# Performance work log

Measured on AMD Instinct MI355X. Metric: run time of the kernel, lower is better.

## Reference

```python
import jax, jax.numpy as jnp
import numpy as np

EPSILON = 0.3
ALPHA = 0.7
LN_EPS = 1e-5


def _layernorm(x, g, b):
    mu = jnp.mean(x, axis=-1, keepdims=True)
    var = jnp.mean((x - mu) ** 2, axis=-1, keepdims=True)
    return (x - mu) / jnp.sqrt(var + LN_EPS) * g + b


def setup_inputs() -> dict:
    key = jax.random.key(0)
    ks = jax.random.split(key, 6)
    B, N, D, L = 1, 2048, 768, 16
    s = 0.05  # weight scale to keep sigmoid/exp well-conditioned
    return {
        "x": jax.random.normal(ks[0], (B, N, D), jnp.float32),
        "proj_w": jax.random.normal(ks[1], (D, L), jnp.float32) * s,
        "proj_b": jnp.zeros((L,), jnp.float32),
        "ln1_g": jnp.ones((L,), jnp.float32),
        "ln1_b": jnp.zeros((L,), jnp.float32),
        "pi_w1": jax.random.normal(ks[2], (L, D), jnp.float32) * s,
        "pi_b1": jnp.zeros((D,), jnp.float32),
        "pi_w2": jax.random.normal(ks[3], (D, 1), jnp.float32) * s,
        "pi_b2": jnp.zeros((1,), jnp.float32),
        "dt": jnp.full((1,), 0.05, jnp.float32),
        "f_w": jax.random.normal(ks[4], (D, D), jnp.float32) * s,
        "f_b": jnp.zeros((D,), jnp.float32),
        "ln2_g": jnp.ones((D,), jnp.float32),
        "ln2_b": jnp.zeros((D,), jnp.float32),
    }


def reference(x, proj_w, proj_b, ln1_g, ln1_b, pi_w1, pi_b1, pi_w2, pi_b2, dt, f_w, f_b, ln2_g, ln2_b):
    B, N, D = x.shape
    # proj_list: Linear -> LayerNorm -> ReLU. [B,N,L]
    x_proj = jax.nn.relu(_layernorm(x @ proj_w + proj_b, ln1_g, ln1_b))
    # RBF kernel over pairwise differences. [B,N,N]
    diff = x_proj[:, :, None, :] - x_proj[:, None, :, :]
    K_eps = jnp.exp(-(1.0 / (4.0 * EPSILON)) * jnp.sum(diff * diff, axis=-1))
    q_tilde = jnp.sum(K_eps, axis=2)  # [B,N]
    # pi_list: Linear -> ReLU -> Linear -> Sigmoid. [B,N]
    pi = jax.nn.sigmoid(jax.nn.relu(x_proj @ pi_w1 + pi_b1) @ pi_w2 + pi_b2)[..., 0]
    v = pi / q_tilde  # diagonal of D_epsilon_tilde
    # K_tilde = K_eps @ diag(v): column scaling (math-equivalent to bmm with diag_embed)
    K_tilde = K_eps * v[:, None, :]
    d = jnp.sum(K_tilde, axis=2) + 1e-5  # diagonal of D_tilde
    # inv(D_tilde) @ K_tilde: row scaling; then subtract identity
    L_op = (1.0 / EPSILON) * (K_tilde / d[:, :, None]) - jnp.eye(N, dtype=x.dtype)[None]
    L_mat = L_op[0]  # .squeeze(0), B == 1
    # f(x): modeled as linear map
    target = x @ f_w + f_b  # [B,N,D]
    tt = dt * jnp.einsum('ij,bjd->bid', L_mat, target)  # target_transformed
    target1 = target + tt
    target2 = ALPHA * x + (1.0 - ALPHA) * (target1 + tt)
    return _layernorm(target2, ln2_g, ln2_b)
```

## Files before the change

kernel.cpp:

```cpp
#include <hip/hip_runtime.h>
#include <math.h>

#define EPSILON 0.3f
#define ALPHA 0.7f
#define LN_EPS 1e-5f

typedef __bf16 bf16x8 __attribute__((ext_vector_type(8)));
typedef float f32x4 __attribute__((ext_vector_type(4)));

__device__ __forceinline__ unsigned short f2bf(float f) {
  unsigned int u = __float_as_uint(f);
  return (unsigned short)((u + 0x7fffu + ((u >> 16) & 1u)) >> 16);
}
__device__ __forceinline__ unsigned int pack2(float lo, float hi) {
  return (unsigned int)f2bf(lo) | ((unsigned int)f2bf(hi) << 16);
}

__device__ __forceinline__ void async16(const unsigned short* g,
                                        unsigned short* l) {
  __builtin_amdgcn_global_load_lds(
      (const __attribute__((address_space(1))) unsigned int*)g,
      (__attribute__((address_space(3))) unsigned int*)l, 16, 0, 0);
}

__device__ __forceinline__ float wave_reduce(float v) {
#pragma unroll
  for (int off = 32; off > 0; off >>= 1) v += __shfl_xor(v, off, 64);
  return v;
}

__device__ __forceinline__ float blk_reduce_sum(float v, float* red) {
  v = wave_reduce(v);
  int lane = threadIdx.x & 63, wid = threadIdx.x >> 6;
  __syncthreads();
  if (lane == 0) red[wid] = v;
  __syncthreads();
  return red[0] + red[1] + red[2] + red[3];
}

__global__ __launch_bounds__(256) void k_proj(
    const float* __restrict__ x, const float* __restrict__ proj_w,
    const float* __restrict__ proj_b, const float* __restrict__ ln1_g,
    const float* __restrict__ ln1_b, const float* __restrict__ pi_w1,
    const float* __restrict__ pi_b1, const float* __restrict__ pi_w2,
    const float* __restrict__ pi_b2, const float* __restrict__ fw,
    unsigned short* __restrict__ fwTb, float* __restrict__ xp,
    float* __restrict__ s, float* __restrict__ pi, int N, int D) {
  __shared__ float xs[16][68];
  __shared__ float ws[64][20];
  __shared__ float ysh[16][17];
  __shared__ float xps[16][16];
  __shared__ float pr[16][4];
  int tid = threadIdx.x;
  int nProj = N / 16;
  if (blockIdx.x >= (unsigned)nProj) {
    unsigned short(*tile)[33] = (unsigned short(*)[33])&ws[0][0];
    int t = blockIdx.x - nProj;
    int tx = tid & 31, ty = tid >> 5;
    int cols = D / 32;
    int c0 = (t % cols) * 32, r0 = (t / cols) * 32;
#pragma unroll
    for (int i = 0; i < 4; ++i) {
      int r = r0 + ty + i * 8;
      tile[ty + i * 8][tx] = f2bf(fw[(size_t)r * D + c0 + tx]);
    }
    __syncthreads();
#pragma unroll
    for (int i = 0; i < 4; ++i) {
      int cc = c0 + ty + i * 8;
      fwTb[(size_t)cc * D + r0 + tx] = tile[tx][ty + i * 8];
    }
    return;
  }
  int row0 = blockIdx.x * 16;
  int row = tid >> 4, l = tid & 15;
  int lane = tid & 63, w = tid >> 6;
  int skc = (tid & 15) * 4;
  int wk = tid >> 2, wl = (tid & 3) * 4;
  float acc = 0.f;
  for (int k0 = 0; k0 < D; k0 += 64) {
    float4 xv = *(const float4*)(x + (size_t)(row0 + row) * D + k0 + skc);
    float4 wv = *(const float4*)(proj_w + (size_t)(k0 + wk) * 16 + wl);
    __syncthreads();
    *(float4*)&xs[row][skc] = xv;
    *(float4*)&ws[wk][wl] = wv;
    __syncthreads();
#pragma unroll
    for (int kk = 0; kk < 64; kk += 4) {
      float4 a4 = *(const float4*)&xs[row][kk];
      acc += a4.x * ws[kk + 0][l];
      acc += a4.y * ws[kk + 1][l];
      acc += a4.z * ws[kk + 2][l];
      acc += a4.w * ws[kk + 3][l];
    }
  }
  float y = acc + proj_b[l];
  ysh[row][l] = y;
  __syncthreads();
  float mu = 0.f;
#pragma unroll
  for (int t = 0; t < 16; ++t) mu += ysh[row][t];
  mu *= (1.f / 16.f);
  float var = 0.f;
#pragma unroll
  for (int t = 0; t < 16; ++t) { float d2 = ysh[row][t] - mu; var += d2 * d2; }
  var *= (1.f / 16.f);
  float rstd = rsqrtf(var + LN_EPS);
  float xpv = fmaxf((y - mu) * rstd * ln1_g[l] + ln1_b[l], 0.f);
  xps[row][l] = xpv;
  xp[(size_t)(row0 + row) * 16 + l] = xpv;
  float sq = xpv * xpv;
  sq += __shfl_xor(sq, 8, 64);
  sq += __shfl_xor(sq, 4, 64);
  sq += __shfl_xor(sq, 2, 64);
  sq += __shfl_xor(sq, 1, 64);
  if ((lane & 15) == 0) s[row0 + row] = sq;
  __syncthreads();
  float w1r[3][16], b1r[3], w2r[3];
#pragma unroll
  for (int c = 0; c < 3; ++c) {
    int d0 = tid + c * 256;
    b1r[c] = pi_b1[d0];
    w2r[c] = pi_w2[d0];
#pragma unroll
    for (int t = 0; t < 16; ++t) w1r[c][t] = pi_w1[(size_t)t * D + d0];
  }
#pragma unroll
  for (int r = 0; r < 16; ++r) {
    float xv[16];
#pragma unroll
    for (int t4 = 0; t4 < 4; ++t4) {
      float4 xq = *(const float4*)&xps[r][t4 * 4];
      xv[t4 * 4 + 0] = xq.x; xv[t4 * 4 + 1] = xq.y;
      xv[t4 * 4 + 2] = xq.z; xv[t4 * 4 + 3] = xq.w;
    }
    float pa = 0.f;
#pragma unroll
    for (int c = 0; c < 3; ++c) {
      float h = b1r[c];
#pragma unroll
      for (int t = 0; t < 16; ++t) h += xv[t] * w1r[c][t];
      h = fmaxf(h, 0.f);
      pa += h * w2r[c];
    }
    float pv = wave_reduce(pa);
    if (lane == 0) pr[r][w] = pv;
  }
  __syncthreads();
  if (tid < 16) {
    float tot = pr[tid][0] + pr[tid][1] + pr[tid][2] + pr[tid][3] + pi_b2[0];
    pi[row0 + tid] = 1.f / (1.f + expf(-tot));
  }
}

__global__ __launch_bounds__(256) void k_keps(
    const float* __restrict__ xp, const float* __restrict__ s,
    const float* __restrict__ pi, unsigned short* __restrict__ Kb,
    float* __restrict__ v, int N) {
  __shared__ float qs[4][4];
  int i0 = blockIdx.x * 4;
  int tid = threadIdx.x, lane = tid & 63, w = tid >> 6;
  float a[4][16], si[4];
#pragma unroll
  for (int r = 0; r < 4; ++r) {
    const float* ap = xp + (size_t)(i0 + r) * 16;
#pragma unroll
    for (int t = 0; t < 16; ++t) a[r][t] = ap[t];
    si[r] = s[i0 + r];
  }
  const float c = 1.f / (4.f * EPSILON);
  float qa[4] = {0.f, 0.f, 0.f, 0.f};
  for (int it = 0; it < N / 512; ++it) {
    int j = it * 512 + tid * 2;
    const float4* bp = (const float4*)(xp + (size_t)j * 16);
    float4 b0 = bp[0], b1 = bp[1], b2 = bp[2], b3 = bp[3];
    float4 c0 = bp[4], c1 = bp[5], c2 = bp[6], c3 = bp[7];
    float bv[16] = {b0.x, b0.y, b0.z, b0.w, b1.x, b1.y, b1.z, b1.w,
                    b2.x, b2.y, b2.z, b2.w, b3.x, b3.y, b3.z, b3.w};
    float cv[16] = {c0.x, c0.y, c0.z, c0.w, c1.x, c1.y, c1.z, c1.w,
                    c2.x, c2.y, c2.z, c2.w, c3.x, c3.y, c3.z, c3.w};
    float sj0 = s[j], sj1 = s[j + 1];
#pragma unroll
    for (int r = 0; r < 4; ++r) {
      float d0 = 0.f, d1 = 0.f;
#pragma unroll
      for (int t = 0; t < 16; ++t) { d0 += a[r][t] * bv[t]; d1 += a[r][t] * cv[t]; }
      float k0 = __expf(-c * (si[r] + sj0 - 2.f * d0));
      float k1 = __expf(-c * (si[r] + sj1 - 2.f * d1));
      *(unsigned int*)(Kb + (size_t)(i0 + r) * N + j) = pack2(k0, k1);
      qa[r] += k0 + k1;
    }
  }
#pragma unroll
  for (int r = 0; r < 4; ++r) {
    float t = wave_reduce(qa[r]);
    if (lane == 0) qs[r][w] = t;
  }
  __syncthreads();
  if (tid < 4) {
    float tot = qs[tid][0] + qs[tid][1] + qs[tid][2] + qs[tid][3];
    v[i0 + tid] = pi[i0 + tid] / tot;
  }
}

__global__ __launch_bounds__(256) void k_prep(
    const unsigned short* __restrict__ Kb, const float* __restrict__ v,
    float* __restrict__ dv, const float* __restrict__ x,
    unsigned short* __restrict__ xvbT, int N, int D) {
  __shared__ float sh[544];
  int bid = blockIdx.x, tid = threadIdx.x;
  if (bid < N) {
    int i = bid;
    float acc = 0.f;
    for (int j8 = tid * 8; j8 < N; j8 += 256 * 8) {
      uint4 kv4 = *(const uint4*)(Kb + (size_t)i * N + j8);
      float4 va = *(const float4*)(v + j8);
      float4 vb = *(const float4*)(v + j8 + 4);
      unsigned int u;
      u = kv4.x;
      acc += __uint_as_float(u << 16) * va.x + __uint_as_float(u & 0xffff0000u) * va.y;
      u = kv4.y;
      acc += __uint_as_float(u << 16) * va.z + __uint_as_float(u & 0xffff0000u) * va.w;
      u = kv4.z;
      acc += __uint_as_float(u << 16) * vb.x + __uint_as_float(u & 0xffff0000u) * vb.y;
      u = kv4.w;
      acc += __uint_as_float(u << 16) * vb.z + __uint_as_float(u & 0xffff0000u) * vb.w;
    }
    float tot = blk_reduce_sum(acc, sh);
    if (tid == 0) dv[i] = tot + 1e-5f;
  } else {
    int t = bid - N;
    unsigned short(*tile)[33] = (unsigned short(*)[33])sh;
    int tx = tid & 31, ty = tid >> 5;
    int cols = D / 32;
    int c0 = (t % cols) * 32;
    int r0 = (t / cols) * 32;
#pragma unroll
    for (int i = 0; i < 4; ++i) {
      int r = r0 + ty + i * 8;
      tile[ty + i * 8][tx] = f2bf(v[r] * x[(size_t)r * D + c0 + tx]);
    }
    __syncthreads();
#pragma unroll
    for (int i = 0; i < 4; ++i) {
      int cc = c0 + ty + i * 8;
      xvbT[(size_t)cc * N + r0 + tx] = tile[tx][ty + i * 8];
    }
  }
}

#define GEMM_KLOOP(Aptr, Bptr, Kdim)                                          \
  int tid = threadIdx.x;                                                      \
  int w = tid >> 6, l = tid & 63;                                             \
  int ln = l & 15, quad = l >> 4;                                             \
  int mh = (w & 1) * 32, nh = (w >> 1) * 32;                                  \
  int row0 = blockIdx.y * 64, col0 = blockIdx.x * 64;                         \
  int srow = w * 4 + (l >> 4);                                                \
  int swz = ((l & 15) ^ srow) * 8;                                            \
  const unsigned short* gA = Aptr + (size_t)(row0 + srow) * Kdim + swz;       \
  const unsigned short* gB = Bptr + (size_t)(col0 + srow) * Kdim + swz;       \
  f32x4 acc[2][2] = {};                                                       \
  for (int k0 = 0; k0 < Kdim; k0 += 128) {                                    \
    __syncthreads();                                                          \
    _Pragma("unroll")                                                         \
    for (int q = 0; q < 4; ++q) {                                             \
      async16(gA + (size_t)q * 16 * Kdim + k0, As + (q * 16 + w * 4) * 128);  \
      async16(gB + (size_t)q * 16 * Kdim + k0, Bs + (q * 16 + w * 4) * 128);  \
    }                                                                         \
    __syncthreads();                                                          \
    _Pragma("unroll")                                                         \
    for (int ks = 0; ks < 4; ++ks) {                                          \
      bf16x8 bfr[2], afr[2];                                                  \
      _Pragma("unroll")                                                       \
      for (int nt = 0; nt < 2; ++nt) {                                        \
        int r = nh + nt * 16 + ln;                                            \
        int cix = (ks * 4 + quad) ^ (r & 15);                                 \
        bfr[nt] = *(const bf16x8*)&Bs[r * 128 + cix * 8];                     \
      }                                                                       \
      _Pragma("unroll")                                                       \
      for (int mt = 0; mt < 2; ++mt) {                                        \
        int r = mh + mt * 16 + ln;                                            \
        int cix = (ks * 4 + quad) ^ (r & 15);                                 \
        afr[mt] = *(const bf16x8*)&As[r * 128 + cix * 8];                     \
      }                                                                       \
      _Pragma("unroll")                                                       \
      for (int mt = 0; mt < 2; ++mt)                                          \
        _Pragma("unroll")                                                     \
        for (int nt = 0; nt < 2; ++nt)                                        \
          acc[mt][nt] = __builtin_amdgcn_mfma_f32_16x16x32_bf16(              \
              afr[mt], bfr[nt], acc[mt][nt], 0, 0, 0);                        \
    }                                                                         \
  }

__global__ __launch_bounds__(256) void k_gemmA(
    const unsigned short* __restrict__ A, const unsigned short* __restrict__ Bt,
    const float* __restrict__ x, const float* __restrict__ dv,
    const float* __restrict__ dtp, unsigned short* __restrict__ Z,
    int M, int N, int K) {
  __shared__ unsigned short As[64 * 128];
  __shared__ unsigned short Bs[64 * 128];
  GEMM_KLOOP(A, Bt, K)
  float dtv = dtp[0];
  float c2 = (1.f - ALPHA) * (1.f - 2.f * dtv);
  float c3b = (1.f - ALPHA) * 2.f * dtv / EPSILON;
#pragma unroll
  for (int mt = 0; mt < 2; ++mt)
#pragma unroll
    for (int nt = 0; nt < 2; ++nt) {
      int col = col0 + nh + nt * 16 + ln;
#pragma unroll
      for (int r = 0; r < 4; ++r) {
        int row = row0 + mh + mt * 16 + quad * 4 + r;
        float c3 = c3b / dv[row];
        Z[(size_t)row * N + col] =
            f2bf(c2 * x[(size_t)row * N + col] + c3 * acc[mt][nt][r]);
      }
    }
}

__global__ __launch_bounds__(256) void k_gemmB(
    const unsigned short* __restrict__ A, const unsigned short* __restrict__ Bt,
    const float* __restrict__ x, const float* __restrict__ bias,
    const float* __restrict__ dtp, float* __restrict__ out,
    int M, int N, int K) {
  __shared__ unsigned short As[64 * 128];
  __shared__ unsigned short Bs[64 * 128];
  GEMM_KLOOP(A, Bt, K)
  float dtv = dtp[0];
  float cb = (1.f - ALPHA) * (1.f - 2.f * dtv) +
             (1.f - ALPHA) * 2.f * dtv / EPSILON;
#pragma unroll
  for (int mt = 0; mt < 2; ++mt)
#pragma unroll
    for (int nt = 0; nt < 2; ++nt) {
      int col = col0 + nh + nt * 16 + ln;
      float bv = cb * bias[col];
#pragma unroll
      for (int r = 0; r < 4; ++r) {
        int row = row0 + mh + mt * 16 + quad * 4 + r;
        size_t idx = (size_t)row * N + col;
        out[idx] = ALPHA * x[idx] + acc[mt][nt][r] + bv;
      }
    }
}

__global__ __launch_bounds__(256) void k_ln_rows(
    float* __restrict__ out, const float* __restrict__ g,
    const float* __restrict__ b, int D) {
  __shared__ float red[4];
  int i = blockIdx.x, tid = threadIdx.x;
  float vv[4];
  int nt = D / 256;
  float sum = 0.f;
  for (int t = 0; t < nt; ++t) {
    vv[t] = out[(size_t)i * D + tid + t * 256];
    sum += vv[t];
  }
  float mu = blk_reduce_sum(sum, red) / (float)D;
  float sq = 0.f;
  for (int t = 0; t < nt; ++t) { float d2 = vv[t] - mu; sq += d2 * d2; }
  float var = blk_reduce_sum(sq, red) / (float)D;
  float rs = rsqrtf(var + LN_EPS);
  for (int t = 0; t < nt; ++t) {
    int d0 = tid + t * 256;
    out[(size_t)i * D + d0] = (vv[t] - mu) * rs * g[d0] + b[d0];
  }
}

extern "C" void kernel_launch(void* const* d_in, const int* in_sizes, int n_in,
                              void* d_out, int out_size, void* d_ws, size_t ws_size,
                              hipStream_t stream) {
  const float* x = (const float*)d_in[0];
  const float* proj_w = (const float*)d_in[1];
  const float* proj_b = (const float*)d_in[2];
  const float* ln1_g = (const float*)d_in[3];
  const float* ln1_b = (const float*)d_in[4];
  const float* pi_w1 = (const float*)d_in[5];
  const float* pi_b1 = (const float*)d_in[6];
  const float* pi_w2 = (const float*)d_in[7];
  const float* pi_b2 = (const float*)d_in[8];
  const float* dt = (const float*)d_in[9];
  const float* f_w = (const float*)d_in[10];
  const float* f_b = (const float*)d_in[11];
  const float* ln2_g = (const float*)d_in[12];
  const float* ln2_b = (const float*)d_in[13];
  float* out = (float*)d_out;

  int D = in_sizes[11];
  int N = in_sizes[0] / D;

  unsigned short* Kb = (unsigned short*)d_ws;
  unsigned short* xvbT = Kb + (size_t)N * N;
  unsigned short* fwTb = xvbT + (size_t)D * N;
  unsigned short* Z = fwTb + (size_t)D * D;
  float* xp = (float*)(Z + (size_t)N * D);
  float* s = xp + (size_t)N * 16;
  float* pi = s + N;
  float* v = pi + N;
  float* dv = v + N;

  int fwB = (D / 32) * (D / 32);
  int xvtB = (D / 32) * (N / 32);

  k_proj<<<N / 16 + fwB, 256, 0, stream>>>(x, proj_w, proj_b, ln1_g, ln1_b,
                                           pi_w1, pi_b1, pi_w2, pi_b2, f_w,
                                           fwTb, xp, s, pi, N, D);
  k_keps<<<N / 4, 256, 0, stream>>>(xp, s, pi, Kb, v, N);
  k_prep<<<N + xvtB, 256, 0, stream>>>(Kb, v, dv, x, xvbT, N, D);
  k_gemmA<<<dim3(D / 64, N / 64), 256, 0, stream>>>(Kb, xvbT, x, dv, dt, Z,
                                                    N, D, N);
  k_gemmB<<<dim3(D / 64, N / 64), 256, 0, stream>>>(Z, fwTb, x, f_b, dt, out,
                                                    N, D, D);
  k_ln_rows<<<N, 256, 0, stream>>>(out, ln2_g, ln2_b, D);
}
```

Before: 158.4 us.

## Fuse six kernels into one persistent cooperative kernel with grid syncs

Replaces the six separate kernel launches with a single cooperative persistent kernel that loops over work items in each stage and separates stages with grid-wide syncs. This removes per-launch overhead and inter-kernel gaps. In exchange, the grid is capped at 512 blocks (bounded by occupancy), so the large stages run in grid-stride loops and may lose parallelism. Grid syncs also add their own cost, and the original kernels are kept as a fallback if the cooperative launch fails.

```diff
diff --git a/kernel.cpp b/kernel.cpp
--- a/kernel.cpp
+++ b/kernel.cpp
@@ -1,5 +1,8 @@
 #include <hip/hip_runtime.h>
+#include <hip/hip_cooperative_groups.h>
 #include <math.h>
+
+namespace cg = cooperative_groups;
 
 #define EPSILON 0.3f
 #define ALPHA 0.7f
@@ -37,6 +40,424 @@
   __syncthreads();
   return red[0] + red[1] + red[2] + red[3];
 }
+
+struct ProjSh {
+  float xs[16][68];
+  float ws[64][20];
+  float ysh[16][17];
+  float xps[16][16];
+  float pr[16][4];
+};
+
+__global__ __launch_bounds__(256) void k_mega(
+    const float* __restrict__ x, const float* __restrict__ proj_w,
+    const float* __restrict__ proj_b, const float* __restrict__ ln1_g,
+    const float* __restrict__ ln1_b, const float* __restrict__ pi_w1,
+    const float* __restrict__ pi_b1, const float* __restrict__ pi_w2,
+    const float* __restrict__ pi_b2, const float* __restrict__ dtp,
+    const float* __restrict__ fw, const float* __restrict__ fb,
+    const float* __restrict__ ln2_g, const float* __restrict__ ln2_b,
+    unsigned short* __restrict__ Kb, unsigned short* __restrict__ xvbT,
+    unsigned short* __restrict__ fwTb, unsigned short* __restrict__ Z,
+    float* __restrict__ xp, float* __restrict__ s, float* __restrict__ pi,
+    float* __restrict__ v, float* __restrict__ dv, float* __restrict__ out,
+    int N, int D) {
+  cg::grid_group gg = cg::this_grid();
+  __shared__ __align__(16) unsigned char pool[32768];
+  __shared__ float qs[4][4];
+  const int tid = threadIdx.x;
+  const int bid = blockIdx.x;
+  const int nBlk = gridDim.x;
+  const int lane = tid & 63, wv = tid >> 6;
+
+  {
+    int nProj = N / 16;
+    int cols = D / 64;
+    int nItems = nProj + cols * cols;
+    for (int item = bid; item < nItems; item += nBlk) {
+      __syncthreads();
+      if (item >= nProj) {
+        int t = item - nProj;
+        unsigned short(*tile)[65] = (unsigned short(*)[65])pool;
+        int c0 = (t % cols) * 64, r0 = (t / cols) * 64;
+#pragma unroll
+        for (int i = 0; i < 16; ++i) {
+          int rr = wv * 16 + i;
+          tile[rr][lane] = f2bf(fw[(size_t)(r0 + rr) * D + c0 + lane]);
+        }
+        __syncthreads();
+#pragma unroll
+        for (int i = 0; i < 16; ++i) {
+          int rr = wv * 16 + i;
+          fwTb[(size_t)(c0 + rr) * D + r0 + lane] = tile[lane][rr];
+        }
+        continue;
+      }
+      ProjSh& P = *(ProjSh*)pool;
+      int row0 = item * 16;
+      int row = tid >> 4, l = tid & 15;
+      int skc = (tid & 15) * 4;
+      int wk = tid >> 2, wl = (tid & 3) * 4;
+      float acc = 0.f;
+      for (int k0 = 0; k0 < D; k0 += 64) {
+        float4 xv = *(const float4*)(x + (size_t)(row0 + row) * D + k0 + skc);
+        float4 wvec = *(const float4*)(proj_w + (size_t)(k0 + wk) * 16 + wl);
+        __syncthreads();
+        *(float4*)&P.xs[row][skc] = xv;
+        *(float4*)&P.ws[wk][wl] = wvec;
+        __syncthreads();
+#pragma unroll
+        for (int kk = 0; kk < 64; kk += 4) {
+          float4 a4 = *(const float4*)&P.xs[row][kk];
+          acc += a4.x * P.ws[kk + 0][l];
+          acc += a4.y * P.ws[kk + 1][l];
+          acc += a4.z * P.ws[kk + 2][l];
+          acc += a4.w * P.ws[kk + 3][l];
+        }
+      }
+      float y = acc + proj_b[l];
+      P.ysh[row][l] = y;
+      __syncthreads();
+      float mu = 0.f;
+#pragma unroll
+      for (int t = 0; t < 16; ++t) mu += P.ysh[row][t];
+      mu *= (1.f / 16.f);
+      float var = 0.f;
+#pragma unroll
+      for (int t = 0; t < 16; ++t) {
+        float d2 = P.ysh[row][t] - mu;
+        var += d2 * d2;
+      }
+      var *= (1.f / 16.f);
+      float rstd = rsqrtf(var + LN_EPS);
+      float xpv = fmaxf((y - mu) * rstd * ln1_g[l] + ln1_b[l], 0.f);
+      P.xps[row][l] = xpv;
+      xp[(size_t)(row0 + row) * 16 + l] = xpv;
+      float sq = xpv * xpv;
+      sq += __shfl_xor(sq, 8, 64);
+      sq += __shfl_xor(sq, 4, 64);
+      sq += __shfl_xor(sq, 2, 64);
+      sq += __shfl_xor(sq, 1, 64);
+      if ((lane & 15) == 0) s[row0 + row] = sq;
+      __syncthreads();
+      float w1r[3][16], b1r[3], w2r[3];
+#pragma unroll
+      for (int c = 0; c < 3; ++c) {
+        int d0 = tid + c * 256;
+        b1r[c] = pi_b1[d0];
+        w2r[c] = pi_w2[d0];
+#pragma unroll
+        for (int t = 0; t < 16; ++t) w1r[c][t] = pi_w1[(size_t)t * D + d0];
+      }
+#pragma unroll
+      for (int r = 0; r < 16; ++r) {
+        float xv2[16];
+#pragma unroll
+        for (int t4 = 0; t4 < 4; ++t4) {
+          float4 xq = *(const float4*)&P.xps[r][t4 * 4];
+          xv2[t4 * 4 + 0] = xq.x;
+          xv2[t4 * 4 + 1] = xq.y;
+          xv2[t4 * 4 + 2] = xq.z;
+          xv2[t4 * 4 + 3] = xq.w;
+        }
+        float pa = 0.f;
+#pragma unroll
+        for (int c = 0; c < 3; ++c) {
+          float h = b1r[c];
+#pragma unroll
+          for (int t = 0; t < 16; ++t) h += xv2[t] * w1r[c][t];
+          h = fmaxf(h, 0.f);
+          pa += h * w2r[c];
+        }
+        float pv = wave_reduce(pa);
+        if (lane == 0) P.pr[r][wv] = pv;
+      }
+      __syncthreads();
+      if (tid < 16) {
+        float tot = P.pr[tid][0] + P.pr[tid][1] + P.pr[tid][2] + P.pr[tid][3] +
+                    pi_b2[0];
+        pi[row0 + tid] = 1.f / (1.f + expf(-tot));
+      }
+    }
+  }
+  __threadfence();
+  gg.sync();
+
+  {
+    int nItems = N / 4;
+    for (int item = bid; item < nItems; item += nBlk) {
+      __syncthreads();
+      int i0 = item * 4;
+      float a[4][16], si[4];
+#pragma unroll
+      for (int r = 0; r < 4; ++r) {
+        const float* ap = xp + (size_t)(i0 + r) * 16;
+#pragma unroll
+        for (int t = 0; t < 16; ++t) a[r][t] = ap[t];
+        si[r] = s[i0 + r];
+      }
+      const float cc = 1.f / (4.f * EPSILON);
+      float qa[4] = {0.f, 0.f, 0.f, 0.f};
+      for (int it = 0; it < N / 512; ++it) {
+        int j = it * 512 + tid * 2;
+        const float4* bp = (const float4*)(xp + (size_t)j * 16);
+        float4 b0 = bp[0], b1 = bp[1], b2 = bp[2], b3 = bp[3];
+        float4 c0 = bp[4], c1 = bp[5], c2 = bp[6], c3 = bp[7];
+        float bvv[16] = {b0.x, b0.y, b0.z, b0.w, b1.x, b1.y, b1.z, b1.w,
+                         b2.x, b2.y, b2.z, b2.w, b3.x, b3.y, b3.z, b3.w};
+        float cvv[16] = {c0.x, c0.y, c0.z, c0.w, c1.x, c1.y, c1.z, c1.w,
+                         c2.x, c2.y, c2.z, c2.w, c3.x, c3.y, c3.z, c3.w};
+        float sj0 = s[j], sj1 = s[j + 1];
+#pragma unroll
+        for (int r = 0; r < 4; ++r) {
+          float d0 = 0.f, d1 = 0.f;
+#pragma unroll
+          for (int t = 0; t < 16; ++t) {
+            d0 += a[r][t] * bvv[t];
+            d1 += a[r][t] * cvv[t];
+          }
+          float k0 = __expf(-cc * (si[r] + sj0 - 2.f * d0));
+          float k1 = __expf(-cc * (si[r] + sj1 - 2.f * d1));
+          *(unsigned int*)(Kb + (size_t)(i0 + r) * N + j) = pack2(k0, k1);
+          qa[r] += k0 + k1;
+        }
+      }
+#pragma unroll
+      for (int r = 0; r < 4; ++r) {
+        float t = wave_reduce(qa[r]);
+        if (lane == 0) qs[r][wv] = t;
+      }
+      __syncthreads();
+      if (tid < 4) {
+        float tot = qs[tid][0] + qs[tid][1] + qs[tid][2] + qs[tid][3];
+        v[i0 + tid] = pi[i0 + tid] / tot;
+      }
+    }
+  }
+  __threadfence();
+  gg.sync();
+
+  {
+    int nDv = N / 4;
+    int cols = D / 64;
+    int nXT = cols * (N / 64);
+    for (int item = bid; item < nDv + nXT; item += nBlk) {
+      if (item < nDv) {
+        int i = item * 4 + wv;
+        const unsigned short* kr = Kb + (size_t)i * N;
+        float acc = 0.f;
+        for (int c0 = lane * 8; c0 < N; c0 += 512) {
+          uint4 kv = *(const uint4*)(kr + c0);
+          float4 va = *(const float4*)(v + c0);
+          float4 vb = *(const float4*)(v + c0 + 4);
+          unsigned int u;
+          u = kv.x;
+          acc += __uint_as_float(u << 16) * va.x +
+                 __uint_as_float(u & 0xffff0000u) * va.y;
+          u = kv.y;
+          acc += __uint_as_float(u << 16) * va.z +
+                 __uint_as_float(u & 0xffff0000u) * va.w;
+          u = kv.z;
+          acc += __uint_as_float(u << 16) * vb.x +
+                 __uint_as_float(u & 0xffff0000u) * vb.y;
+          u = kv.w;
+          acc += __uint_as_float(u << 16) * vb.z +
+                 __uint_as_float(u & 0xffff0000u) * vb.w;
+        }
+        acc = wave_reduce(acc);
+        if (lane == 0) dv[i] = acc + 1e-5f;
+      } else {
+        int t = item - nDv;
+        __syncthreads();
+        unsigned short(*tile)[65] = (unsigned short(*)[65])pool;
+        int c0 = (t % cols) * 64, r0 = (t / cols) * 64;
+#pragma unroll
+        for (int i = 0; i < 16; ++i) {
+          int rr = wv * 16 + i;
+          tile[rr][lane] =
+              f2bf(v[r0 + rr] * x[(size_t)(r0 + rr) * D + c0 + lane]);
+        }
+        __syncthreads();
+#pragma unroll
+        for (int i = 0; i < 16; ++i) {
+          int rr = wv * 16 + i;
+          xvbT[(size_t)(c0 + rr) * N + r0 + lane] = tile[lane][rr];
+        }
+      }
+    }
+  }
+  __threadfence();
+  gg.sync();
+
+  {
+    float dtv = dtp[0];
+    float c2 = (1.f - ALPHA) * (1.f - 2.f * dtv);
+    float c3b = (1.f - ALPHA) * 2.f * dtv / EPSILON;
+    unsigned short* As = (unsigned short*)pool;
+    unsigned short* Bs = As + 64 * 128;
+    int tilesX = D / 64;
+    int nT = tilesX * (N / 64);
+    int ln = lane & 15, quad = lane >> 4;
+    int mh = (wv & 1) * 32, nh = (wv >> 1) * 32;
+    int srow = wv * 4 + quad;
+    int swz = (ln ^ srow) * 8;
+    for (int item = bid; item < nT; item += nBlk) {
+      int row0 = (item / tilesX) * 64, col0 = (item % tilesX) * 64;
+      const unsigned short* gA = Kb + (size_t)(row0 + srow) * N + swz;
+      const unsigned short* gB = xvbT + (size_t)(col0 + srow) * N + swz;
+      f32x4 acc[2][2] = {};
+      for (int k0 = 0; k0 < N; k0 += 128) {
+        __syncthreads();
+#pragma unroll
+        for (int q = 0; q < 4; ++q) {
+          async16(gA + (size_t)q * 16 * N + k0, As + (q * 16 + wv * 4) * 128);
+          async16(gB + (size_t)q * 16 * N + k0, Bs + (q * 16 + wv * 4) * 128);
+        }
+        __syncthreads();
+#pragma unroll
+        for (int ks = 0; ks < 4; ++ks) {
+          bf16x8 bfr[2], afr[2];
+#pragma unroll
+          for (int nt = 0; nt < 2; ++nt) {
+            int r = nh + nt * 16 + ln;
+            int cix = (ks * 4 + quad) ^ (r & 15);
+            bfr[nt] = *(const bf16x8*)&Bs[r * 128 + cix * 8];
+          }
+#pragma unroll
+          for (int mt = 0; mt < 2; ++mt) {
+            int r = mh + mt * 16 + ln;
+            int cix = (ks * 4 + quad) ^ (r & 15);
+            afr[mt] = *(const bf16x8*)&As[r * 128 + cix * 8];
+          }
+#pragma unroll
+          for (int mt = 0; mt < 2; ++mt)
+#pragma unroll
+            for (int nt = 0; nt < 2; ++nt)
+              acc[mt][nt] = __builtin_amdgcn_mfma_f32_16x16x32_bf16(
+                  afr[mt], bfr[nt], acc[mt][nt], 0, 0, 0);
+        }
+      }
+#pragma unroll
+      for (int mt = 0; mt < 2; ++mt)
+#pragma unroll
+        for (int nt = 0; nt < 2; ++nt) {
+          int col = col0 + nh + nt * 16 + ln;
+#pragma unroll
+          for (int r = 0; r < 4; ++r) {
+            int row = row0 + mh + mt * 16 + quad * 4 + r;
+            float c3 = c3b / dv[row];
+            Z[(size_t)row * D + col] =
+                f2bf(c2 * x[(size_t)row * D + col] + c3 * acc[mt][nt][r]);
+          }
+        }
+    }
+  }
+  __threadfence();
+  gg.sync();
+
+  {
+    float dtv = dtp[0];
+    float cb = (1.f - ALPHA) * (1.f - 2.f * dtv) +
+               (1.f - ALPHA) * 2.f * dtv / EPSILON;
+    unsigned short* As = (unsigned short*)pool;
+    unsigned short* Bs = As + 64 * 128;
+    int tilesX = D / 64;
+    int nT = tilesX * (N / 64);
+    int ln = lane & 15, quad = lane >> 4;
+    int mh = (wv & 1) * 32, nh = (wv >> 1) * 32;
+    int srow = wv * 4 + quad;
+    int swz = (ln ^ srow) * 8;
+    for (int item = bid; item < nT; item += nBlk) {
+      int row0 = (item / tilesX) * 64, col0 = (item % tilesX) * 64;
+      const unsigned short* gA = Z + (size_t)(row0 + srow) * D + swz;
+      const unsigned short* gB = fwTb + (size_t)(col0 + srow) * D + swz;
+      f32x4 acc[2][2] = {};
+      for (int k0 = 0; k0 < D; k0 += 128) {
+        __syncthreads();
+#pragma unroll
+        for (int q = 0; q < 4; ++q) {
+          async16(gA + (size_t)q * 16 * D + k0, As + (q * 16 + wv * 4) * 128);
+          async16(gB + (size_t)q * 16 * D + k0, Bs + (q * 16 + wv * 4) * 128);
+        }
+        __syncthreads();
+#pragma unroll
+        for (int ks = 0; ks < 4; ++ks) {
+          bf16x8 bfr[2], afr[2];
+#pragma unroll
+          for (int nt = 0; nt < 2; ++nt) {
+            int r = nh + nt * 16 + ln;
+            int cix = (ks * 4 + quad) ^ (r & 15);
+            bfr[nt] = *(const bf16x8*)&Bs[r * 128 + cix * 8];
+          }
+#pragma unroll
+          for (int mt = 0; mt < 2; ++mt) {
+            int r = mh + mt * 16 + ln;
+            int cix = (ks * 4 + quad) ^ (r & 15);
+            afr[mt] = *(const bf16x8*)&As[r * 128 + cix * 8];
+          }
+#pragma unroll
+          for (int mt = 0; mt < 2; ++mt)
+#pragma unroll
+            for (int nt = 0; nt < 2; ++nt)
+              acc[mt][nt] = __builtin_amdgcn_mfma_f32_16x16x32_bf16(
+                  afr[mt], bfr[nt], acc[mt][nt], 0, 0, 0);
+        }
+      }
+#pragma unroll
+      for (int mt = 0; mt < 2; ++mt)
+#pragma unroll
+        for (int nt = 0; nt < 2; ++nt) {
+          int col = col0 + nh + nt * 16 + ln;
+          float bv = cb * fb[col];
+#pragma unroll
+          for (int r = 0; r < 4; ++r) {
+            int row = row0 + mh + mt * 16 + quad * 4 + r;
+            size_t idx = (size_t)row * D + col;
+            out[idx] = ALPHA * x[idx] + acc[mt][nt][r] + bv;
+          }
+        }
+    }
+  }
+  __threadfence();
+  gg.sync();
+
+  {
+    int nItems = N / 4;
+    for (int item = bid; item < nItems; item += nBlk) {
+      int i = item * 4 + wv;
+      float4 vv[3];
+      float sum = 0.f;
+#pragma unroll
+      for (int t = 0; t < 3; ++t) {
+        vv[t] = *(const float4*)(out + (size_t)i * D + lane * 4 + t * 256);
+        sum += vv[t].x + vv[t].y + vv[t].z + vv[t].w;
+      }
+      float mu = wave_reduce(sum) / (float)D;
+      float sq = 0.f;
+#pragma unroll
+      for (int t = 0; t < 3; ++t) {
+        float dx = vv[t].x - mu, dy = vv[t].y - mu;
+        float dz = vv[t].z - mu, dw = vv[t].w - mu;
+        sq += dx * dx + dy * dy + dz * dz + dw * dw;
+      }
+      float var = wave_reduce(sq) / (float)D;
+      float rs = rsqrtf(var + LN_EPS);
+#pragma unroll
+      for (int t = 0; t < 3; ++t) {
+        int d0 = lane * 4 + t * 256;
+        float4 gv = *(const float4*)(ln2_g + d0);
+        float4 bv = *(const float4*)(ln2_b + d0);
+        float4 o;
+        o.x = (vv[t].x - mu) * rs * gv.x + bv.x;
+        o.y = (vv[t].y - mu) * rs * gv.y + bv.y;
+        o.z = (vv[t].z - mu) * rs * gv.z + bv.z;
+        o.w = (vv[t].w - mu) * rs * gv.w + bv.w;
+        *(float4*)(out + (size_t)i * D + d0) = o;
+      }
+    }
+  }
+}
+
 
 __global__ __launch_bounds__(256) void k_proj(
     const float* __restrict__ x, const float* __restrict__ proj_w,
@@ -399,17 +820,41 @@
   float* v = pi + N;
   float* dv = v + N;
 
-  int fwB = (D / 32) * (D / 32);
-  int xvtB = (D / 32) * (N / 32);
-
-  k_proj<<<N / 16 + fwB, 256, 0, stream>>>(x, proj_w, proj_b, ln1_g, ln1_b,
-                                           pi_w1, pi_b1, pi_w2, pi_b2, f_w,
-                                           fwTb, xp, s, pi, N, D);
-  k_keps<<<N / 4, 256, 0, stream>>>(xp, s, pi, Kb, v, N);
-  k_prep<<<N + xvtB, 256, 0, stream>>>(Kb, v, dv, x, xvbT, N, D);
-  k_gemmA<<<dim3(D / 64, N / 64), 256, 0, stream>>>(Kb, xvbT, x, dv, dt, Z,
-                                                    N, D, N);
-  k_gemmB<<<dim3(D / 64, N / 64), 256, 0, stream>>>(Z, fwTb, x, f_b, dt, out,
-                                                    N, D, D);
-  k_ln_rows<<<N, 256, 0, stream>>>(out, ln2_g, ln2_b, D);
-}
+  bool ok = false;
+  int maxBlk = 0;
+  hipError_t qerr =
+      hipOccupancyMaxActiveBlocksPerMultiprocessor(&maxBlk, k_mega, 256, 0);
+  if (qerr == hipSuccess && maxBlk > 0) {
+    int dev = 0, numCU = 256;
+    hipGetDevice(&dev);
+    hipDeviceGetAttribute(&numCU, hipDeviceAttributeMultiprocessorCount, dev);
+    long cap = (long)maxBlk * (long)numCU;
+    int grid = (int)(cap < 512 ? cap : 512);
+    void* kargs[] = {(void*)&x,     (void*)&proj_w, (void*)&proj_b,
+                     (void*)&ln1_g, (void*)&ln1_b,  (void*)&pi_w1,
+                     (void*)&pi_b1, (void*)&pi_w2,  (void*)&pi_b2,
+                     (void*)&dt,    (void*)&f_w,    (void*)&f_b,
+                     (void*)&ln2_g, (void*)&ln2_b,  (void*)&Kb,
+                     (void*)&xvbT,  (void*)&fwTb,   (void*)&Z,
+                     (void*)&xp,    (void*)&s,      (void*)&pi,
+                     (void*)&v,     (void*)&dv,     (void*)&out,
+                     (void*)&N,     (void*)&D};
+    ok = hipLaunchCooperativeKernel((const void*)k_mega, dim3(grid), dim3(256),
+                                    kargs, 0, stream) == hipSuccess;
+  }
+
+  if (!ok) {
+    int fwB = (D / 32) * (D / 32);
+    int xvtB = (D / 32) * (N / 32);
+    k_proj<<<N / 16 + fwB, 256, 0, stream>>>(x, proj_w, proj_b, ln1_g, ln1_b,
+                                             pi_w1, pi_b1, pi_w2, pi_b2, f_w,
+                                             fwTb, xp, s, pi, N, D);
+    k_keps<<<N / 4, 256, 0, stream>>>(xp, s, pi, Kb, v, N);
+    k_prep<<<N + xvtB, 256, 0, stream>>>(Kb, v, dv, x, xvbT, N, D);
+    k_gemmA<<<dim3(D / 64, N / 64), 256, 0, stream>>>(Kb, xvbT, x, dv, dt, Z,
+                                                      N, D, N);
+    k_gemmB<<<dim3(D / 64, N / 64), 256, 0, stream>>>(Z, fwTb, x, f_b, dt, out,
+                                                      N, D, D);
+    k_ln_rows<<<N, 256, 0, stream>>>(out, ln2_g, ln2_b, D);
+  }
+}
```

Result: no change. 159.0 us (+0.4%).
